# Kernel optimization log

Hardware: AMD Instinct MI355X
Metric: run time of the kernel (lower is better)

The kernel has to match this reference:

```python
import jax, jax.numpy as jnp
import numpy as np
import math

D_MODEL = 1024
NHEAD = 16
D_K = D_MODEL // NHEAD
B, S = 2, 2048


def setup_inputs() -> dict:
    key = jax.random.key(0)
    ks = jax.random.split(key, 9)
    x = jax.random.normal(ks[0], (B, S, D_MODEL), dtype=jnp.float32)
    # causal mask, broadcastable to (B, nhead, S, S); 0 entries are masked out
    mask = jnp.tril(jnp.ones((S, S), dtype=jnp.int32))[None, None, :, :]
    scale = 1.0 / math.sqrt(D_MODEL)
    def lin(kw, kb):
        W = jax.random.uniform(kw, (D_MODEL, D_MODEL), dtype=jnp.float32, minval=-scale, maxval=scale)
        b = jax.random.uniform(kb, (D_MODEL,), dtype=jnp.float32, minval=-scale, maxval=scale)
        return W, b
    Wq, bq = lin(ks[1], ks[2])
    Wk, bk = lin(ks[3], ks[4])
    Wv, bv = lin(ks[5], ks[6])
    Wo, bo = lin(ks[7], ks[8])
    return {"x": x, "mask": mask, "Wq": Wq, "bq": bq, "Wk": Wk, "bk": bk,
            "Wv": Wv, "bv": bv, "Wo": Wo, "bo": bo}


def reference(x, mask, Wq, bq, Wk, bk, Wv, bv, Wo, bo):
    b, s, _ = x.shape
    def heads(W, bias):
        # (b, s, d_model) @ (d_model, d_model) -> (b, nhead, s, d_k)
        return (x @ W.T + bias).reshape(b, s, NHEAD, D_K).transpose(0, 2, 1, 3)
    Q, K, V = heads(Wq, bq), heads(Wk, bk), heads(Wv, bv)
    scores = jnp.einsum('bhqd,bhkd->bhqk', Q, K) / math.sqrt(D_K)
    scores = jnp.where(mask == 0, jnp.float32(-1e9), scores)
    attn = jax.nn.softmax(scores, axis=-1)  # dropout is identity in eval mode
    out = jnp.einsum('bhqk,bhkd->bhqd', attn, V)
    out = out.transpose(0, 2, 1, 3).reshape(b, s, D_MODEL)
    return out @ Wo.T + bo
```

## Files before the change

### kernel.cpp

```cpp
#include <hip/hip_runtime.h>
#include <hip/hip_bf16.h>

#define DMODEL 1024
#define NH     16
#define DKH    64
#define BSZ    2
#define SEQ    2048
#define MROWS  (BSZ*SEQ)
#define WELEM  (DMODEL*DMODEL)

typedef __attribute__((ext_vector_type(8))) short short8;
typedef __attribute__((ext_vector_type(4))) short short4v;
typedef __attribute__((ext_vector_type(4))) float f32x4;

__device__ __forceinline__ f32x4 mfma_pv16(short4v a, short4v b, f32x4 c) {
#if defined(__HIP_DEVICE_COMPILE__)
#if __has_builtin(__builtin_amdgcn_mfma_f32_16x16x16bf16_1k)
    return __builtin_amdgcn_mfma_f32_16x16x16bf16_1k(a, b, c, 0, 0, 0);
#elif __has_builtin(__builtin_amdgcn_mfma_f32_16x16x16_bf16)
    return __builtin_amdgcn_mfma_f32_16x16x16_bf16(a, b, c, 0, 0, 0);
#else
    f32x4 d;
    asm volatile("v_mfma_f32_16x16x16_bf16 %0, %1, %2, %3"
                 : "=v"(d) : "v"(a), "v"(b), "v"(c));
    return d;
#endif
#else
    (void)a; (void)b;
    return c;
#endif
}

__device__ __forceinline__ ushort f2bf(float f) {
    return __bfloat16_as_ushort(__float2bfloat16(f));
}
__device__ __forceinline__ unsigned pk2(float lo, float hi) {
    return (unsigned)f2bf(lo) | ((unsigned)f2bf(hi) << 16);
}
__device__ __forceinline__ void load_lds16(const ushort* g, ushort* l) {
    __builtin_amdgcn_global_load_lds(
        (const __attribute__((address_space(1))) unsigned int*)g,
        (__attribute__((address_space(3))) unsigned int*)l, 16, 0, 0);
}

__global__ __launch_bounds__(256)
void cvt_all(const float* __restrict__ x,
             const float* __restrict__ W0, const float* __restrict__ W1,
             const float* __restrict__ W2, const float* __restrict__ W3,
             ushort* __restrict__ xbf, ushort* __restrict__ Wcat,
             ushort* __restrict__ Wo)
{
    const int blk = blockIdx.x;
    const float* src;
    ushort* dst;
    int base;
    if (blk < 2048)      { src = x;  dst = xbf;             base = blk * 2048; }
    else if (blk < 2560) { src = W0; dst = Wcat;            base = (blk - 2048) * 2048; }
    else if (blk < 3072) { src = W1; dst = Wcat + WELEM;    base = (blk - 2560) * 2048; }
    else if (blk < 3584) { src = W2; dst = Wcat + 2*WELEM;  base = (blk - 3072) * 2048; }
    else                 { src = W3; dst = Wo;              base = (blk - 3584) * 2048; }
    const size_t off = (size_t)base + threadIdx.x * 8;
    const float4 f0 = *(const float4*)(src + off);
    const float4 f1 = *(const float4*)(src + off + 4);
    uint4 o;
    o.x = pk2(f0.x, f0.y); o.y = pk2(f0.z, f0.w);
    o.z = pk2(f1.x, f1.y); o.w = pk2(f1.z, f1.w);
    *(uint4*)(dst + off) = o;
}

__global__ __launch_bounds__(256)
void gemm_qkv(const ushort* __restrict__ xbf, const ushort* __restrict__ Wcat,
              const float* __restrict__ bq, const float* __restrict__ bk,
              const float* __restrict__ bv,
              ushort* __restrict__ Qh, ushort* __restrict__ Kh,
              ushort* __restrict__ VT)
{
    __shared__ ushort Ash[128][32];
    __shared__ ushort Bsh[128][32];

    const int t    = threadIdx.x;
    const int m0   = blockIdx.y * 128, n0 = blockIdx.x * 128;
    const int wave = t >> 6;
    const int lane = t & 63;
    const int wr   = (wave >> 1) * 64;
    const int wc   = (wave & 1) * 64;
    const int quad = lane >> 4;
    const int r16  = lane & 15;

    const int row0 = wave * 16 + (lane >> 2);
    const int row1 = 64 + wave * 16 + (lane >> 2);
    const int ch   = (lane & 3) * 8;

    f32x4 acc[4][4];
    #pragma unroll
    for (int i = 0; i < 4; ++i)
        #pragma unroll
        for (int j = 0; j < 4; ++j)
            acc[i][j] = (f32x4){0.f, 0.f, 0.f, 0.f};

    for (int k0 = 0; k0 < DMODEL; k0 += 32) {
        load_lds16(xbf  + (size_t)(m0 + row0) * DMODEL + k0 + ch, &Ash[wave * 16][0]);
        load_lds16(xbf  + (size_t)(m0 + row1) * DMODEL + k0 + ch, &Ash[64 + wave * 16][0]);
        load_lds16(Wcat + (size_t)(n0 + row0) * DMODEL + k0 + ch, &Bsh[wave * 16][0]);
        load_lds16(Wcat + (size_t)(n0 + row1) * DMODEL + k0 + ch, &Bsh[64 + wave * 16][0]);
        __syncthreads();

        short8 af[4], bf[4];
        #pragma unroll
        for (int i = 0; i < 4; ++i) af[i] = *(const short8*)&Ash[wr + i * 16 + r16][quad * 8];
        #pragma unroll
        for (int j = 0; j < 4; ++j) bf[j] = *(const short8*)&Bsh[wc + j * 16 + r16][quad * 8];

        #pragma unroll
        for (int i = 0; i < 4; ++i)
            #pragma unroll
            for (int j = 0; j < 4; ++j)
                acc[i][j] = __builtin_amdgcn_mfma_f32_16x16x32_bf16(af[i], bf[j], acc[i][j], 0, 0, 0);
        __syncthreads();
    }

    const int region = n0 >> 10;
    const float* bp  = (region == 0) ? bq : (region == 1) ? bk : bv;
    ushort* outQK    = (region == 0) ? Qh : Kh;
    const float osc  = (region == 0) ? 0.18033688f : 1.0f;
    const int nbase  = n0 & 1023;

    #pragma unroll
    for (int i = 0; i < 4; ++i) {
        #pragma unroll
        for (int j = 0; j < 4; ++j) {
            #pragma unroll
            for (int reg = 0; reg < 4; ++reg) {
                const int m  = m0 + wr + i * 16 + quad * 4 + reg;
                const int n  = nbase + wc + j * 16 + r16;
                const float v = (acc[i][j][reg] + bp[n]) * osc;
                const int b = m >> 11, s = m & (SEQ - 1);
                const int h = n >> 6,  dk = n & 63;
                if (region < 2) {
                    outQK[((size_t)(b * NH + h) * SEQ + s) * DKH + dk] = f2bf(v);
                } else {
                    VT[(((size_t)(b * NH + h)) * DKH + dk) * SEQ + s] = f2bf(v);
                }
            }
        }
    }
}

__global__ __launch_bounds__(256)
void gemm_out(const ushort* __restrict__ O, const ushort* __restrict__ Wo,
              const float* __restrict__ bo, float* __restrict__ out)
{
    __shared__ ushort Ash[128][32];
    __shared__ ushort Bsh[64][32];

    const int t    = threadIdx.x;
    const int m0   = blockIdx.y * 128, n0 = blockIdx.x * 64;
    const int wave = t >> 6;
    const int lane = t & 63;
    const int wr   = (wave >> 1) * 64;
    const int wc   = (wave & 1) * 32;
    const int quad = lane >> 4;
    const int r16  = lane & 15;

    const int row0 = wave * 16 + (lane >> 2);
    const int row1 = 64 + wave * 16 + (lane >> 2);
    const int ch   = (lane & 3) * 8;

    f32x4 acc[4][2];
    #pragma unroll
    for (int i = 0; i < 4; ++i)
        #pragma unroll
        for (int j = 0; j < 2; ++j)
            acc[i][j] = (f32x4){0.f, 0.f, 0.f, 0.f};

    for (int k0 = 0; k0 < DMODEL; k0 += 32) {
        const int ma0 = m0 + row0, ma1 = m0 + row1;
        load_lds16(O + ((size_t)(ma0 >> 11) * NH + (k0 >> 6)) * (SEQ * DKH)
                     + (size_t)(ma0 & (SEQ - 1)) * DKH + (k0 & 63) + ch,
                   &Ash[wave * 16][0]);
        load_lds16(O + ((size_t)(ma1 >> 11) * NH + (k0 >> 6)) * (SEQ * DKH)
                     + (size_t)(ma1 & (SEQ - 1)) * DKH + (k0 & 63) + ch,
                   &Ash[64 + wave * 16][0]);
        load_lds16(Wo + (size_t)(n0 + row0) * DMODEL + k0 + ch, &Bsh[wave * 16][0]);
        __syncthreads();

        short8 af[4], bf[2];
        #pragma unroll
        for (int i = 0; i < 4; ++i) af[i] = *(const short8*)&Ash[wr + i * 16 + r16][quad * 8];
        #pragma unroll
        for (int j = 0; j < 2; ++j) bf[j] = *(const short8*)&Bsh[wc + j * 16 + r16][quad * 8];

        #pragma unroll
        for (int i = 0; i < 4; ++i)
            #pragma unroll
            for (int j = 0; j < 2; ++j)
                acc[i][j] = __builtin_amdgcn_mfma_f32_16x16x32_bf16(af[i], bf[j], acc[i][j], 0, 0, 0);
        __syncthreads();
    }

    #pragma unroll
    for (int i = 0; i < 4; ++i) {
        #pragma unroll
        for (int j = 0; j < 2; ++j) {
            #pragma unroll
            for (int reg = 0; reg < 4; ++reg) {
                const int m = m0 + wr + i * 16 + quad * 4 + reg;
                const int n = n0 + wc + j * 16 + r16;
                out[(size_t)m * DMODEL + n] = acc[i][j][reg] + bo[n];
            }
        }
    }
}

__global__ __launch_bounds__(256)
void gemm_mfma(const void* __restrict__ A, const void* __restrict__ W,
               const float* __restrict__ bias, void* __restrict__ out,
               int amode, int bmode, int outmode, float oscale)
{
    __shared__ ushort Ash[128][40];
    __shared__ ushort Bsh[128][40];

    const int t    = threadIdx.x;
    const int m0   = blockIdx.y * 128, n0 = blockIdx.x * 128;
    const int srow = t >> 1;
    const int shal = (t & 1) * 16;

    const int wave = t >> 6;
    const int lane = t & 63;
    const int wr   = (wave >> 1) * 64;
    const int wc   = (wave & 1) * 64;
    const int quad = lane >> 4;
    const int r16  = lane & 15;

    f32x4 acc[4][4];
    #pragma unroll
    for (int i = 0; i < 4; ++i)
        #pragma unroll
        for (int j = 0; j < 4; ++j)
            acc[i][j] = (f32x4){0.f, 0.f, 0.f, 0.f};

    for (int k0 = 0; k0 < DMODEL; k0 += 32) {
        uint4 a01, a23, b01, b23;
        if (amode == 0) {
            const float* ap = (const float*)A + (size_t)(m0 + srow) * DMODEL + k0 + shal;
            const float4 f0 = *(const float4*)(ap);
            const float4 f1 = *(const float4*)(ap + 4);
            const float4 f2 = *(const float4*)(ap + 8);
            const float4 f3 = *(const float4*)(ap + 12);
            a01 = (uint4){pk2(f0.x,f0.y), pk2(f0.z,f0.w), pk2(f1.x,f1.y), pk2(f1.z,f1.w)};
            a23 = (uint4){pk2(f2.x,f2.y), pk2(f2.z,f2.w), pk2(f3.x,f3.y), pk2(f3.z,f3.w)};
        } else if (amode == 1) {
            const int m = m0 + srow;
            const ushort* ap = (const ushort*)A
                + ((size_t)(m >> 11) * NH + (k0 >> 6)) * (SEQ * DKH)
                + (size_t)(m & (SEQ - 1)) * DKH + (k0 & 63) + shal;
            a01 = *(const uint4*)(ap);
            a23 = *(const uint4*)(ap + 8);
        } else {
            const ushort* ap = (const ushort*)A + (size_t)(m0 + srow) * DMODEL + k0 + shal;
            a01 = *(const uint4*)(ap);
            a23 = *(const uint4*)(ap + 8);
        }
        if (bmode == 0) {
            const float* wp = (const float*)W + (size_t)(n0 + srow) * DMODEL + k0 + shal;
            const float4 w0 = *(const float4*)(wp);
            const float4 w1 = *(const float4*)(wp + 4);
            const float4 w2 = *(const float4*)(wp + 8);
            const float4 w3 = *(const float4*)(wp + 12);
            b01 = (uint4){pk2(w0.x,w0.y), pk2(w0.z,w0.w), pk2(w1.x,w1.y), pk2(w1.z,w1.w)};
            b23 = (uint4){pk2(w2.x,w2.y), pk2(w2.z,w2.w), pk2(w3.x,w3.y), pk2(w3.z,w3.w)};
        } else {
            const ushort* wp = (const ushort*)W + (size_t)(n0 + srow) * DMODEL + k0 + shal;
            b01 = *(const uint4*)(wp);
            b23 = *(const uint4*)(wp + 8);
        }

        *(uint4*)&Ash[srow][shal]     = a01;
        *(uint4*)&Ash[srow][shal + 8] = a23;
        *(uint4*)&Bsh[srow][shal]     = b01;
        *(uint4*)&Bsh[srow][shal + 8] = b23;
        __syncthreads();

        short8 af[4], bf[4];
        #pragma unroll
        for (int i = 0; i < 4; ++i) af[i] = *(const short8*)&Ash[wr + i * 16 + r16][quad * 8];
        #pragma unroll
        for (int j = 0; j < 4; ++j) bf[j] = *(const short8*)&Bsh[wc + j * 16 + r16][quad * 8];

        #pragma unroll
        for (int i = 0; i < 4; ++i)
            #pragma unroll
            for (int j = 0; j < 4; ++j)
                acc[i][j] = __builtin_amdgcn_mfma_f32_16x16x32_bf16(af[i], bf[j], acc[i][j], 0, 0, 0);
        __syncthreads();
    }

    #pragma unroll
    for (int i = 0; i < 4; ++i) {
        #pragma unroll
        for (int j = 0; j < 4; ++j) {
            #pragma unroll
            for (int reg = 0; reg < 4; ++reg) {
                const int m = m0 + wr + i * 16 + quad * 4 + reg;
                const int n = n0 + wc + j * 16 + r16;
                const float v = (acc[i][j][reg] + bias[n]) * oscale;
                if (outmode == 0) {
                    ((float*)out)[(size_t)m * DMODEL + n] = v;
                } else if (outmode == 1) {
                    ((ushort*)out)[((size_t)(m >> 11) * NH + (n >> 6)) * (SEQ * DKH)
                                   + (size_t)(m & (SEQ - 1)) * DKH + (n & 63)] = f2bf(v);
                } else {
                    ((ushort*)out)[(((size_t)(m >> 11) * NH + (n >> 6)) * DKH + (n & 63)) * SEQ
                                   + (m & (SEQ - 1))] = f2bf(v);
                }
            }
        }
    }
}

__global__ __launch_bounds__(512, 4)
void attn_flash(ushort* __restrict__ Qh,
                const ushort* __restrict__ Kh,
                const ushort* __restrict__ VT)
{
    __shared__ ushort Kl[128][72];
    __shared__ ushort Vl[64][136];

    const int t512 = threadIdx.x;
    const int wave = t512 >> 6;
    const int lane = t512 & 63;
    const int quad = lane >> 4;
    const int r16  = lane & 15;

    const int slot = blockIdx.x & 7;
    const int bh   = slot * 4 + ((blockIdx.x >> 3) & 3);
    const int qt   = 15 - (blockIdx.x >> 5);
    const int q0   = qt * 128;

    ushort*       Qbase = Qh + (size_t)bh * SEQ * DKH;
    const ushort* Kbase = Kh + (size_t)bh * SEQ * DKH;
    const ushort* Vbase = VT + (size_t)bh * DKH * SEQ;

    short8 qf[2];
    {
        const ushort* qrow = Qbase + (size_t)(q0 + wave * 16 + r16) * DKH;
        qf[0] = *(const short8*)(qrow + quad * 8);
        qf[1] = *(const short8*)(qrow + 32 + quad * 8);
    }

    f32x4 oacc[4];
    #pragma unroll
    for (int i = 0; i < 4; ++i) oacc[i] = (f32x4){0.f, 0.f, 0.f, 0.f};
    f32x4 lsum4 = (f32x4){0.f, 0.f, 0.f, 0.f};

    const int T    = qt + 1;
    const int qrel = wave * 16 + r16;

    const int krow = t512 >> 2, kc = (t512 & 3) * 16;
    const int vrow = t512 >> 3, vc = (t512 & 7) * 16;
    const ushort* kg0 = Kbase + (size_t)krow * DKH + kc;
    const ushort* vg0 = Vbase + (size_t)vrow * SEQ + vc;

    uint4 kr0, kr1, vr0, vr1;
    kr0 = *(const uint4*)(kg0);
    kr1 = *(const uint4*)(kg0 + 8);
    vr0 = *(const uint4*)(vg0);
    vr1 = *(const uint4*)(vg0 + 8);

    for (int t = 0; t < T - 1; ++t) {
        *(uint4*)&Kl[krow][kc]     = kr0;
        *(uint4*)&Kl[krow][kc + 8] = kr1;
        *(uint4*)&Vl[vrow][vc]     = vr0;
        *(uint4*)&Vl[vrow][vc + 8] = vr1;
        __syncthreads();

        {
            const ushort* kg = kg0 + (size_t)(t + 1) * 128 * DKH;
            kr0 = *(const uint4*)(kg);
            kr1 = *(const uint4*)(kg + 8);
            const ushort* vg = vg0 + (size_t)(t + 1) * 128;
            vr0 = *(const uint4*)(vg);
            vr1 = *(const uint4*)(vg + 8);
        }

        #pragma unroll
        for (int nt = 0; nt < 8; ++nt) {
            short8 b0 = *(const short8*)&Kl[nt * 16 + r16][quad * 8];
            short8 b1 = *(const short8*)&Kl[nt * 16 + r16][32 + quad * 8];
            f32x4 s = (f32x4){0.f, 0.f, 0.f, 0.f};
            __builtin_amdgcn_s_setprio(1);
            s = __builtin_amdgcn_mfma_f32_16x16x32_bf16(b0, qf[0], s, 0, 0, 0);
            s = __builtin_amdgcn_mfma_f32_16x16x32_bf16(b1, qf[1], s, 0, 0, 0);
            __builtin_amdgcn_s_setprio(0);

            const float e0 = __builtin_amdgcn_exp2f(s[0]);
            const float e1 = __builtin_amdgcn_exp2f(s[1]);
            const float e2 = __builtin_amdgcn_exp2f(s[2]);
            const float e3 = __builtin_amdgcn_exp2f(s[3]);
            lsum4 += (f32x4){e0, e1, e2, e3};
            union { uint2 u; short4v s4; } pw;
            pw.u.x = pk2(e0, e1);
            pw.u.y = pk2(e2, e3);

            __builtin_amdgcn_s_setprio(1);
            #pragma unroll
            for (int ct = 0; ct < 4; ++ct) {
                short4v vb = *(const short4v*)&Vl[ct * 16 + r16][nt * 16 + quad * 4];
                oacc[ct] = mfma_pv16(pw.s4, vb, oacc[ct]);
            }
            __builtin_amdgcn_s_setprio(0);
        }
        __syncthreads();
    }

    {
        *(uint4*)&Kl[krow][kc]     = kr0;
        *(uint4*)&Kl[krow][kc + 8] = kr1;
        *(uint4*)&Vl[vrow][vc]     = vr0;
        *(uint4*)&Vl[vrow][vc + 8] = vr1;
        __syncthreads();

        const int ntmax = wave | 1;

        #pragma unroll
        for (int nt = 0; nt < 8; ++nt) {
            if (nt <= ntmax) {
                short8 b0 = *(const short8*)&Kl[nt * 16 + r16][quad * 8];
                short8 b1 = *(const short8*)&Kl[nt * 16 + r16][32 + quad * 8];
                f32x4 s = (f32x4){0.f, 0.f, 0.f, 0.f};
                __builtin_amdgcn_s_setprio(1);
                s = __builtin_amdgcn_mfma_f32_16x16x32_bf16(b0, qf[0], s, 0, 0, 0);
                s = __builtin_amdgcn_mfma_f32_16x16x32_bf16(b1, qf[1], s, 0, 0, 0);
                __builtin_amdgcn_s_setprio(0);

                float e0 = __builtin_amdgcn_exp2f(s[0]);
                float e1 = __builtin_amdgcn_exp2f(s[1]);
                float e2 = __builtin_amdgcn_exp2f(s[2]);
                float e3 = __builtin_amdgcn_exp2f(s[3]);
                const int kbase = nt * 16 + quad * 4;
                if (kbase + 0 > qrel) e0 = 0.f;
                if (kbase + 1 > qrel) e1 = 0.f;
                if (kbase + 2 > qrel) e2 = 0.f;
                if (kbase + 3 > qrel) e3 = 0.f;
                lsum4 += (f32x4){e0, e1, e2, e3};
                union { uint2 u; short4v s4; } pw;
                pw.u.x = pk2(e0, e1);
                pw.u.y = pk2(e2, e3);

                __builtin_amdgcn_s_setprio(1);
                #pragma unroll
                for (int ct = 0; ct < 4; ++ct) {
                    short4v vb = *(const short4v*)&Vl[ct * 16 + r16][nt * 16 + quad * 4];
                    oacc[ct] = mfma_pv16(pw.s4, vb, oacc[ct]);
                }
                __builtin_amdgcn_s_setprio(0);
            }
        }
    }

    float lsum = (lsum4[0] + lsum4[1]) + (lsum4[2] + lsum4[3]);
    lsum += __shfl_xor(lsum, 16, 64);
    lsum += __shfl_xor(lsum, 32, 64);

    #pragma unroll
    for (int reg = 0; reg < 4; ++reg) {
        const float inv = 1.f / __shfl(lsum, quad * 4 + reg, 64);
        const int q = q0 + wave * 16 + quad * 4 + reg;
        ushort* orow = Qbase + (size_t)q * DKH;
        #pragma unroll
        for (int ct = 0; ct < 4; ++ct)
            orow[ct * 16 + r16] = f2bf(oacc[ct][reg] * inv);
    }
}

extern "C" void kernel_launch(void* const* d_in, const int* in_sizes, int n_in,
                              void* d_out, int out_size, void* d_ws, size_t ws_size,
                              hipStream_t stream)
{
    const float* x  = (const float*)d_in[0];
    const float* Wf[4] = {(const float*)d_in[2], (const float*)d_in[4],
                          (const float*)d_in[6], (const float*)d_in[8]};
    const float* Bf[4] = {(const float*)d_in[3], (const float*)d_in[5],
                          (const float*)d_in[7], (const float*)d_in[9]};

    const size_t HSZ = (size_t)MROWS * DMODEL;
    ushort* Qh = (ushort*)d_ws;
    ushort* Kh = (ushort*)d_out;
    ushort* VT = (ushort*)d_out + HSZ;

    const dim3 blk(256);

    if (ws_size >= 24u * 1024 * 1024) {
        ushort* Wcat = Qh + HSZ;
        ushort* Wo   = Wcat + 3 * (size_t)WELEM;
        ushort* xbf  = Wo + WELEM;

        cvt_all<<<dim3(4096), blk, 0, stream>>>(x, Wf[0], Wf[1], Wf[2], Wf[3],
                                                xbf, Wcat, Wo);

        gemm_qkv<<<dim3(3 * DMODEL / 128, MROWS / 128), blk, 0, stream>>>(
            xbf, Wcat, Bf[0], Bf[1], Bf[2], Qh, Kh, VT);

        attn_flash<<<dim3(BSZ * NH * 16), dim3(512), 0, stream>>>(Qh, Kh, VT);

        gemm_out<<<dim3(DMODEL / 64, MROWS / 128), blk, 0, stream>>>(
            Qh, Wo, Bf[3], (float*)d_out);
    } else {
        const dim3 gg(DMODEL / 128, MROWS / 128);
        gemm_mfma<<<gg, blk, 0, stream>>>(x, Wf[0], Bf[0], Qh, 0, 0, 1, 0.18033688f);
        gemm_mfma<<<gg, blk, 0, stream>>>(x, Wf[1], Bf[1], Kh, 0, 0, 1, 1.0f);
        gemm_mfma<<<gg, blk, 0, stream>>>(x, Wf[2], Bf[2], VT, 0, 0, 2, 1.0f);
        attn_flash<<<dim3(BSZ * NH * 16), dim3(512), 0, stream>>>(Qh, Kh, VT);
        gemm_mfma<<<gg, blk, 0, stream>>>(Qh, Wf[3], Bf[3], d_out, 1, 0, 0, 1.0f);
    }
}
```

Baseline: 197.1 us.

## Process two query row groups per wave in flash attention to reuse K/V fragments

The attention block drops from 8 waves to 4. Each wave now handles 32 query rows as two 16-row groups, so every K and V fragment read from LDS is used by two QK and PV MFMA chains. This halves the LDS reads per MFMA and gives more independent MFMA work per wave. In exchange it doubles the accumulator registers, halves the waves per block, and makes each thread stage twice as many K/V tile bytes. The launch bounds change to 256 threads with 3 blocks, which could lower occupancy.

```diff
diff --git a/kernel.cpp b/kernel.cpp
--- a/kernel.cpp
+++ b/kernel.cpp
@@ -318,7 +318,7 @@
     }
 }
 
-__global__ __launch_bounds__(512, 4)
+__global__ __launch_bounds__(256, 3)
 void attn_flash(ushort* __restrict__ Qh,
                 const ushort* __restrict__ Kh,
                 const ushort* __restrict__ VT)
@@ -326,9 +326,9 @@
     __shared__ ushort Kl[128][72];
     __shared__ ushort Vl[64][136];
 
-    const int t512 = threadIdx.x;
-    const int wave = t512 >> 6;
-    const int lane = t512 & 63;
+    const int t256 = threadIdx.x;
+    const int wave = t256 >> 6;
+    const int lane = t256 & 63;
     const int quad = lane >> 4;
     const int r16  = lane & 15;
 
@@ -341,135 +341,171 @@
     const ushort* Kbase = Kh + (size_t)bh * SEQ * DKH;
     const ushort* Vbase = VT + (size_t)bh * DKH * SEQ;
 
-    short8 qf[2];
-    {
-        const ushort* qrow = Qbase + (size_t)(q0 + wave * 16 + r16) * DKH;
-        qf[0] = *(const short8*)(qrow + quad * 8);
-        qf[1] = *(const short8*)(qrow + 32 + quad * 8);
-    }
-
-    f32x4 oacc[4];
-    #pragma unroll
-    for (int i = 0; i < 4; ++i) oacc[i] = (f32x4){0.f, 0.f, 0.f, 0.f};
-    f32x4 lsum4 = (f32x4){0.f, 0.f, 0.f, 0.f};
-
-    const int T    = qt + 1;
-    const int qrel = wave * 16 + r16;
-
-    const int krow = t512 >> 2, kc = (t512 & 3) * 16;
-    const int vrow = t512 >> 3, vc = (t512 & 7) * 16;
+    short8 qf[2][2];
+    #pragma unroll
+    for (int g = 0; g < 2; ++g) {
+        const ushort* qrow = Qbase + (size_t)(q0 + wave * 32 + g * 16 + r16) * DKH;
+        qf[g][0] = *(const short8*)(qrow + quad * 8);
+        qf[g][1] = *(const short8*)(qrow + 32 + quad * 8);
+    }
+
+    f32x4 oacc[2][4];
+    #pragma unroll
+    for (int g = 0; g < 2; ++g)
+        #pragma unroll
+        for (int i = 0; i < 4; ++i) oacc[g][i] = (f32x4){0.f, 0.f, 0.f, 0.f};
+    f32x4 lsum4[2] = {(f32x4){0.f,0.f,0.f,0.f}, (f32x4){0.f,0.f,0.f,0.f}};
+
+    const int T = qt + 1;
+
+    const int krow = t256 >> 1, kc = (t256 & 1) * 32;
+    const int vrow = t256 >> 2, vc = (t256 & 3) * 32;
     const ushort* kg0 = Kbase + (size_t)krow * DKH + kc;
     const ushort* vg0 = Vbase + (size_t)vrow * SEQ + vc;
 
-    uint4 kr0, kr1, vr0, vr1;
+    uint4 kr0, kr1, kr2, kr3, vr0, vr1, vr2, vr3;
     kr0 = *(const uint4*)(kg0);
     kr1 = *(const uint4*)(kg0 + 8);
+    kr2 = *(const uint4*)(kg0 + 16);
+    kr3 = *(const uint4*)(kg0 + 24);
     vr0 = *(const uint4*)(vg0);
     vr1 = *(const uint4*)(vg0 + 8);
+    vr2 = *(const uint4*)(vg0 + 16);
+    vr3 = *(const uint4*)(vg0 + 24);
 
     for (int t = 0; t < T - 1; ++t) {
-        *(uint4*)&Kl[krow][kc]     = kr0;
-        *(uint4*)&Kl[krow][kc + 8] = kr1;
-        *(uint4*)&Vl[vrow][vc]     = vr0;
-        *(uint4*)&Vl[vrow][vc + 8] = vr1;
+        *(uint4*)&Kl[krow][kc]      = kr0;
+        *(uint4*)&Kl[krow][kc + 8]  = kr1;
+        *(uint4*)&Kl[krow][kc + 16] = kr2;
+        *(uint4*)&Kl[krow][kc + 24] = kr3;
+        *(uint4*)&Vl[vrow][vc]      = vr0;
+        *(uint4*)&Vl[vrow][vc + 8]  = vr1;
+        *(uint4*)&Vl[vrow][vc + 16] = vr2;
+        *(uint4*)&Vl[vrow][vc + 24] = vr3;
         __syncthreads();
 
         {
             const ushort* kg = kg0 + (size_t)(t + 1) * 128 * DKH;
             kr0 = *(const uint4*)(kg);
             kr1 = *(const uint4*)(kg + 8);
+            kr2 = *(const uint4*)(kg + 16);
+            kr3 = *(const uint4*)(kg + 24);
             const ushort* vg = vg0 + (size_t)(t + 1) * 128;
             vr0 = *(const uint4*)(vg);
             vr1 = *(const uint4*)(vg + 8);
+            vr2 = *(const uint4*)(vg + 16);
+            vr3 = *(const uint4*)(vg + 24);
         }
 
         #pragma unroll
         for (int nt = 0; nt < 8; ++nt) {
             short8 b0 = *(const short8*)&Kl[nt * 16 + r16][quad * 8];
             short8 b1 = *(const short8*)&Kl[nt * 16 + r16][32 + quad * 8];
-            f32x4 s = (f32x4){0.f, 0.f, 0.f, 0.f};
-            __builtin_amdgcn_s_setprio(1);
-            s = __builtin_amdgcn_mfma_f32_16x16x32_bf16(b0, qf[0], s, 0, 0, 0);
-            s = __builtin_amdgcn_mfma_f32_16x16x32_bf16(b1, qf[1], s, 0, 0, 0);
-            __builtin_amdgcn_s_setprio(0);
-
-            const float e0 = __builtin_amdgcn_exp2f(s[0]);
-            const float e1 = __builtin_amdgcn_exp2f(s[1]);
-            const float e2 = __builtin_amdgcn_exp2f(s[2]);
-            const float e3 = __builtin_amdgcn_exp2f(s[3]);
-            lsum4 += (f32x4){e0, e1, e2, e3};
-            union { uint2 u; short4v s4; } pw;
-            pw.u.x = pk2(e0, e1);
-            pw.u.y = pk2(e2, e3);
-
-            __builtin_amdgcn_s_setprio(1);
-            #pragma unroll
-            for (int ct = 0; ct < 4; ++ct) {
-                short4v vb = *(const short4v*)&Vl[ct * 16 + r16][nt * 16 + quad * 4];
-                oacc[ct] = mfma_pv16(pw.s4, vb, oacc[ct]);
-            }
-            __builtin_amdgcn_s_setprio(0);
-        }
-        __syncthreads();
-    }
-
-    {
-        *(uint4*)&Kl[krow][kc]     = kr0;
-        *(uint4*)&Kl[krow][kc + 8] = kr1;
-        *(uint4*)&Vl[vrow][vc]     = vr0;
-        *(uint4*)&Vl[vrow][vc + 8] = vr1;
-        __syncthreads();
-
-        const int ntmax = wave | 1;
-
-        #pragma unroll
-        for (int nt = 0; nt < 8; ++nt) {
-            if (nt <= ntmax) {
-                short8 b0 = *(const short8*)&Kl[nt * 16 + r16][quad * 8];
-                short8 b1 = *(const short8*)&Kl[nt * 16 + r16][32 + quad * 8];
+            short4v vb0 = *(const short4v*)&Vl[ 0 + r16][nt * 16 + quad * 4];
+            short4v vb1 = *(const short4v*)&Vl[16 + r16][nt * 16 + quad * 4];
+            short4v vb2 = *(const short4v*)&Vl[32 + r16][nt * 16 + quad * 4];
+            short4v vb3 = *(const short4v*)&Vl[48 + r16][nt * 16 + quad * 4];
+
+            #pragma unroll
+            for (int g = 0; g < 2; ++g) {
                 f32x4 s = (f32x4){0.f, 0.f, 0.f, 0.f};
                 __builtin_amdgcn_s_setprio(1);
-                s = __builtin_amdgcn_mfma_f32_16x16x32_bf16(b0, qf[0], s, 0, 0, 0);
-                s = __builtin_amdgcn_mfma_f32_16x16x32_bf16(b1, qf[1], s, 0, 0, 0);
+                s = __builtin_amdgcn_mfma_f32_16x16x32_bf16(b0, qf[g][0], s, 0, 0, 0);
+                s = __builtin_amdgcn_mfma_f32_16x16x32_bf16(b1, qf[g][1], s, 0, 0, 0);
                 __builtin_amdgcn_s_setprio(0);
 
-                float e0 = __builtin_amdgcn_exp2f(s[0]);
-                float e1 = __builtin_amdgcn_exp2f(s[1]);
-                float e2 = __builtin_amdgcn_exp2f(s[2]);
-                float e3 = __builtin_amdgcn_exp2f(s[3]);
-                const int kbase = nt * 16 + quad * 4;
-                if (kbase + 0 > qrel) e0 = 0.f;
-                if (kbase + 1 > qrel) e1 = 0.f;
-                if (kbase + 2 > qrel) e2 = 0.f;
-                if (kbase + 3 > qrel) e3 = 0.f;
-                lsum4 += (f32x4){e0, e1, e2, e3};
+                const float e0 = __builtin_amdgcn_exp2f(s[0]);
+                const float e1 = __builtin_amdgcn_exp2f(s[1]);
+                const float e2 = __builtin_amdgcn_exp2f(s[2]);
+                const float e3 = __builtin_amdgcn_exp2f(s[3]);
+                lsum4[g] += (f32x4){e0, e1, e2, e3};
                 union { uint2 u; short4v s4; } pw;
                 pw.u.x = pk2(e0, e1);
                 pw.u.y = pk2(e2, e3);
 
                 __builtin_amdgcn_s_setprio(1);
-                #pragma unroll
-                for (int ct = 0; ct < 4; ++ct) {
-                    short4v vb = *(const short4v*)&Vl[ct * 16 + r16][nt * 16 + quad * 4];
-                    oacc[ct] = mfma_pv16(pw.s4, vb, oacc[ct]);
-                }
+                oacc[g][0] = mfma_pv16(pw.s4, vb0, oacc[g][0]);
+                oacc[g][1] = mfma_pv16(pw.s4, vb1, oacc[g][1]);
+                oacc[g][2] = mfma_pv16(pw.s4, vb2, oacc[g][2]);
+                oacc[g][3] = mfma_pv16(pw.s4, vb3, oacc[g][3]);
                 __builtin_amdgcn_s_setprio(0);
             }
         }
-    }
-
-    float lsum = (lsum4[0] + lsum4[1]) + (lsum4[2] + lsum4[3]);
-    lsum += __shfl_xor(lsum, 16, 64);
-    lsum += __shfl_xor(lsum, 32, 64);
-
-    #pragma unroll
-    for (int reg = 0; reg < 4; ++reg) {
-        const float inv = 1.f / __shfl(lsum, quad * 4 + reg, 64);
-        const int q = q0 + wave * 16 + quad * 4 + reg;
-        ushort* orow = Qbase + (size_t)q * DKH;
-        #pragma unroll
-        for (int ct = 0; ct < 4; ++ct)
-            orow[ct * 16 + r16] = f2bf(oacc[ct][reg] * inv);
+        __syncthreads();
+    }
+
+    {
+        *(uint4*)&Kl[krow][kc]      = kr0;
+        *(uint4*)&Kl[krow][kc + 8]  = kr1;
+        *(uint4*)&Kl[krow][kc + 16] = kr2;
+        *(uint4*)&Kl[krow][kc + 24] = kr3;
+        *(uint4*)&Vl[vrow][vc]      = vr0;
+        *(uint4*)&Vl[vrow][vc + 8]  = vr1;
+        *(uint4*)&Vl[vrow][vc + 16] = vr2;
+        *(uint4*)&Vl[vrow][vc + 24] = vr3;
+        __syncthreads();
+
+        #pragma unroll
+        for (int nt = 0; nt < 8; ++nt) {
+            if (nt <= wave * 2 + 1) {
+                short8 b0 = *(const short8*)&Kl[nt * 16 + r16][quad * 8];
+                short8 b1 = *(const short8*)&Kl[nt * 16 + r16][32 + quad * 8];
+                short4v vb0 = *(const short4v*)&Vl[ 0 + r16][nt * 16 + quad * 4];
+                short4v vb1 = *(const short4v*)&Vl[16 + r16][nt * 16 + quad * 4];
+                short4v vb2 = *(const short4v*)&Vl[32 + r16][nt * 16 + quad * 4];
+                short4v vb3 = *(const short4v*)&Vl[48 + r16][nt * 16 + quad * 4];
+                const int kbase = nt * 16 + quad * 4;
+
+                #pragma unroll
+                for (int g = 0; g < 2; ++g) {
+                    if (nt <= wave * 2 + g) {
+                        const int qrel = wave * 32 + g * 16 + r16;
+                        f32x4 s = (f32x4){0.f, 0.f, 0.f, 0.f};
+                        __builtin_amdgcn_s_setprio(1);
+                        s = __builtin_amdgcn_mfma_f32_16x16x32_bf16(b0, qf[g][0], s, 0, 0, 0);
+                        s = __builtin_amdgcn_mfma_f32_16x16x32_bf16(b1, qf[g][1], s, 0, 0, 0);
+                        __builtin_amdgcn_s_setprio(0);
+
+                        float e0 = __builtin_amdgcn_exp2f(s[0]);
+                        float e1 = __builtin_amdgcn_exp2f(s[1]);
+                        float e2 = __builtin_amdgcn_exp2f(s[2]);
+                        float e3 = __builtin_amdgcn_exp2f(s[3]);
+                        if (kbase + 0 > qrel) e0 = 0.f;
+                        if (kbase + 1 > qrel) e1 = 0.f;
+                        if (kbase + 2 > qrel) e2 = 0.f;
+                        if (kbase + 3 > qrel) e3 = 0.f;
+                        lsum4[g] += (f32x4){e0, e1, e2, e3};
+                        union { uint2 u; short4v s4; } pw;
+                        pw.u.x = pk2(e0, e1);
+                        pw.u.y = pk2(e2, e3);
+
+                        __builtin_amdgcn_s_setprio(1);
+                        oacc[g][0] = mfma_pv16(pw.s4, vb0, oacc[g][0]);
+                        oacc[g][1] = mfma_pv16(pw.s4, vb1, oacc[g][1]);
+                        oacc[g][2] = mfma_pv16(pw.s4, vb2, oacc[g][2]);
+                        oacc[g][3] = mfma_pv16(pw.s4, vb3, oacc[g][3]);
+                        __builtin_amdgcn_s_setprio(0);
+                    }
+                }
+            }
+        }
+    }
+
+    #pragma unroll
+    for (int g = 0; g < 2; ++g) {
+        float lsum = (lsum4[g][0] + lsum4[g][1]) + (lsum4[g][2] + lsum4[g][3]);
+        lsum += __shfl_xor(lsum, 16, 64);
+        lsum += __shfl_xor(lsum, 32, 64);
+
+        #pragma unroll
+        for (int reg = 0; reg < 4; ++reg) {
+            const float inv = 1.f / __shfl(lsum, quad * 4 + reg, 64);
+            const int q = q0 + wave * 32 + g * 16 + quad * 4 + reg;
+            ushort* orow = Qbase + (size_t)q * DKH;
+            #pragma unroll
+            for (int ct = 0; ct < 4; ++ct)
+                orow[ct * 16 + r16] = f2bf(oacc[g][ct][reg] * inv);
+        }
     }
 }
 
@@ -501,7 +537,7 @@
         gemm_qkv<<<dim3(3 * DMODEL / 128, MROWS / 128), blk, 0, stream>>>(
             xbf, Wcat, Bf[0], Bf[1], Bf[2], Qh, Kh, VT);
 
-        attn_flash<<<dim3(BSZ * NH * 16), dim3(512), 0, stream>>>(Qh, Kh, VT);
+        attn_flash<<<dim3(BSZ * NH * 16), dim3(256), 0, stream>>>(Qh, Kh, VT);
 
         gemm_out<<<dim3(DMODEL / 64, MROWS / 128), blk, 0, stream>>>(
             Qh, Wo, Bf[3], (float*)d_out);
@@ -510,7 +546,7 @@
         gemm_mfma<<<gg, blk, 0, stream>>>(x, Wf[0], Bf[0], Qh, 0, 0, 1, 0.18033688f);
         gemm_mfma<<<gg, blk, 0, stream>>>(x, Wf[1], Bf[1], Kh, 0, 0, 1, 1.0f);
         gemm_mfma<<<gg, blk, 0, stream>>>(x, Wf[2], Bf[2], VT, 0, 0, 2, 1.0f);
-        attn_flash<<<dim3(BSZ * NH * 16), dim3(512), 0, stream>>>(Qh, Kh, VT);
+        attn_flash<<<dim3(BSZ * NH * 16), dim3(256), 0, stream>>>(Qh, Kh, VT);
         gemm_mfma<<<gg, blk, 0, stream>>>(Qh, Wf[3], Bf[3], d_out, 1, 0, 0, 1.0f);
     }
 }
```

Result: no change. 198.3 us (+0.6%).
